# Performance work log

Measured on AMD Instinct MI355X. Metric: run time of the kernel, lower is better.

Reference implementation:

```python
import jax, jax.numpy as jnp
import numpy as np


def setup_inputs() -> dict:
    key = jax.random.key(0)
    kq, kk, kv = jax.random.split(key, 3)
    B, H, S, D = 2, 8, 4096, 64
    return {
        "query": jax.random.normal(kq, (B, H, S, D), dtype=jnp.float32),
        "key": jax.random.normal(kk, (B, H, S, D), dtype=jnp.float32),
        "value": jax.random.normal(kv, (B, H, S, D), dtype=jnp.float32),
    }


def reference(query, key, value):
    # NOTE: the torch source overwrites sqrt(d) with d, so the divisor is D, not sqrt(D).
    d = query.shape[-1]
    # score: [B, H, S_q, S_k]
    score = jnp.einsum("bhqd,bhkd->bhqk", query, key) / d
    relu = jax.nn.relu(score)  # no softmax / row normalization
    out = jnp.einsum("bhqk,bhkd->bhqd", relu, value)
    return out
```

## Files before the change

### kernel.cpp

```cpp
#include <hip/hip_runtime.h>
#include <hip/hip_bf16.h>
#include <stdint.h>


#define NH 16
#define SEQ 4096
#define DD 64
#define HE (SEQ*DD)
#define HB (HE*2)
#define Q16_OFF 0
#define K16_OFF (NH*HB)
#define V16_OFF (2*NH*HB)
#define WS_NEED (3*NH*HB)

typedef __attribute__((ext_vector_type(8)))  short    bf16x8;
typedef __attribute__((ext_vector_type(16))) float    f32x16;
typedef __attribute__((ext_vector_type(4)))  uint32_t u32x4;

__device__ inline uint32_t f2bf1(float f) {
  return (uint32_t)__builtin_bit_cast(unsigned short, __float2bfloat16(f));
}
__device__ inline uint32_t pack2bf(float a, float b) {
  return f2bf1(a) | (f2bf1(b) << 16);
}
__device__ inline uint32_t relu2(uint32_t w) {
  uint32_t r;
  asm("v_pk_max_f16 %0, %1, 0" : "=v"(r) : "v"(w));
  return r;
}

__global__ __launch_bounds__(256) void prepass_kernel(const float* __restrict__ Q,
                                                      const float* __restrict__ K,
                                                      const float* __restrict__ V,
                                                      char* __restrict__ ws) {
  __shared__ float vt[64*65];
  int bx = blockIdx.x, tid = threadIdx.x;
  if (bx < 2048) {
    size_t base = ((size_t)bx*256 + tid)*8;
    const float4* s = (const float4*)(Q + base);
    float4 a = s[0], b = s[1];
    const float sc = 1.0f/64.0f;
    u32x4 o;
    o.x = pack2bf(a.x*sc, a.y*sc);
    o.y = pack2bf(a.z*sc, a.w*sc);
    o.z = pack2bf(b.x*sc, b.y*sc);
    o.w = pack2bf(b.z*sc, b.w*sc);
    *(u32x4*)(ws + Q16_OFF + base*2) = o;
  } else if (bx < 3072) {
    int tile = bx - 2048;
    int head = tile >> 6, t = tile & 63;
    int r = tid >> 2, c0 = (tid & 3) * 16;
    const float4* s4 = (const float4*)(K + (size_t)head*HE + ((size_t)(t*64 + r))*64 + c0);
    float4 f0 = s4[0], f1 = s4[1], f2 = s4[2], f3 = s4[3];
    u32x4 c_lo, c_hi;
    c_lo.x = pack2bf(f0.x, f0.y); c_lo.y = pack2bf(f0.z, f0.w);
    c_lo.z = pack2bf(f1.x, f1.y); c_lo.w = pack2bf(f1.z, f1.w);
    c_hi.x = pack2bf(f2.x, f2.y); c_hi.y = pack2bf(f2.z, f2.w);
    c_hi.z = pack2bf(f3.x, f3.y); c_hi.w = pack2bf(f3.z, f3.w);
    char* tb = ws + K16_OFF + ((size_t)head*64 + t)*8192;
    int sw = (r & 7) << 4;
    *(u32x4*)(tb + r*128 + ((c0*2)      ^ sw)) = c_lo;
    *(u32x4*)(tb + r*128 + ((c0*2 + 16) ^ sw)) = c_hi;
  } else {
    int tile = bx - 3072;
    int head = tile >> 6, t = tile & 63;
    int k = tid >> 2, c0 = (tid & 3)*16;
    const float4* s4 = (const float4*)(V + (size_t)head*HE + ((size_t)(t*64 + k))*64 + c0);
    float4 f0 = s4[0], f1 = s4[1], f2 = s4[2], f3 = s4[3];
    float tmp[16] = {f0.x,f0.y,f0.z,f0.w, f1.x,f1.y,f1.z,f1.w,
                     f2.x,f2.y,f2.z,f2.w, f3.x,f3.y,f3.z,f3.w};
    #pragma unroll
    for (int j = 0; j < 16; ++j) vt[k*65 + c0 + j] = tmp[j];
    __syncthreads();
    int d = tid >> 2, k0 = (tid & 3)*16;
    float v2[16];
    #pragma unroll
    for (int j = 0; j < 16; ++j) v2[j] = vt[(k0 + j)*65 + d];
    u32x4 c_lo, c_hi;
    c_lo.x = pack2bf(v2[0],  v2[1]);  c_lo.y = pack2bf(v2[2],  v2[3]);
    c_lo.z = pack2bf(v2[4],  v2[5]);  c_lo.w = pack2bf(v2[6],  v2[7]);
    c_hi.x = pack2bf(v2[8],  v2[9]);  c_hi.y = pack2bf(v2[10], v2[11]);
    c_hi.z = pack2bf(v2[12], v2[13]); c_hi.w = pack2bf(v2[14], v2[15]);
    char* tb = ws + V16_OFF + ((size_t)head*64 + t)*8192;
    int sw = (d & 7) << 4;
    *(u32x4*)(tb + d*128 + ((k0*2)      ^ sw)) = c_lo;
    *(u32x4*)(tb + d*128 + ((k0*2 + 16) ^ sw)) = c_hi;
  }
}

__global__ __launch_bounds__(512, 4) void attn_kernel(const char* __restrict__ ws,
                                                      float* __restrict__ out) {
  __shared__ __align__(16) char lds[2*2*16384];
  int bx = blockIdx.x;
  int head = bx >> 5, qblk = bx & 31;
  int tid = threadIdx.x;
  int lane = tid & 63, w = tid >> 6;
  int l31 = lane & 31, h = lane >> 5;
  int g  = w >> 2;
  int wq = w & 3;
  int t2 = tid & 255;

  const char* q16 = ws + Q16_OFF + (size_t)head*HB;
  const char* k16 = ws + K16_OFF + (size_t)head*HB;
  const char* v16 = ws + V16_OFF + (size_t)head*HB;
  int qrow0 = qblk*128 + wq*32;

  bf16x8 qf[4];
  #pragma unroll
  for (int t = 0; t < 4; ++t)
    qf[t] = *(const bf16x8*)(q16 + ((size_t)(qrow0 + l31)*64 + t*16 + h*8)*2);

  f32x16 kZero;
  #pragma unroll
  for (int i = 0; i < 16; ++i) kZero[i] = 0.f;

  f32x16 o[2];
  #pragma unroll
  for (int nd = 0; nd < 2; ++nd)
    #pragma unroll
    for (int i = 0; i < 16; ++i) o[nd][i] = 0.f;

  char* ldsg = lds + g*32768;

  auto stage = [&](int cur, int kt) {
    const char* ktile = k16 + (size_t)(g*32 + kt)*8192;
    const char* vtile = v16 + (size_t)(g*32 + kt)*8192;
    char* lk = ldsg + cur*16384;
    char* lv = lk + 8192;
    #pragma unroll
    for (int c = 0; c < 2; ++c) {
      int off = c*4096 + t2*16;
      __builtin_amdgcn_global_load_lds(
          (const __attribute__((address_space(1))) void*)(ktile + off),
          (__attribute__((address_space(3))) void*)(lk + off), 16, 0, 0);
      __builtin_amdgcn_global_load_lds(
          (const __attribute__((address_space(1))) void*)(vtile + off),
          (__attribute__((address_space(3))) void*)(lv + off), 16, 0, 0);
    }
  };

  auto compute = [&](int cur) {
    const char* lk = ldsg + cur*16384;
    const char* lv = lk + 8192;
    f32x16 st[2];
    #pragma unroll
    for (int n = 0; n < 2; ++n) {
      bf16x8 kf[4];
      int row = n*32 + l31;
      int sw = (row & 7) << 4;
      #pragma unroll
      for (int t = 0; t < 4; ++t)
        kf[t] = *(const bf16x8*)(lk + row*128 + ((t*32 + h*16) ^ sw));
      __builtin_amdgcn_s_setprio(1);
      f32x16 acc = __builtin_amdgcn_mfma_f32_32x32x16_bf16(kf[0], qf[0], kZero, 0, 0, 0);
      #pragma unroll
      for (int t = 1; t < 4; ++t)
        acc = __builtin_amdgcn_mfma_f32_32x32x16_bf16(kf[t], qf[t], acc, 0, 0, 0);
      st[n] = acc;
      __builtin_amdgcn_s_setprio(0);
    }
    bf16x8 vf[2][4];
    #pragma unroll
    for (int nd = 0; nd < 2; ++nd) {
      int row = nd*32 + l31;
      int sw = (row & 7) << 4;
      #pragma unroll
      for (int ks = 0; ks < 4; ++ks)
        vf[nd][ks] = *(const bf16x8*)(lv + row*128 + ((ks*32 + h*16) ^ sw));
    }
    bf16x8 pa[4];
    #pragma unroll
    for (int n = 0; n < 2; ++n)
      #pragma unroll
      for (int kn = 0; kn < 2; ++kn) {
        uint32_t a0 = pack2bf(st[n][kn*8+0], st[n][kn*8+1]);
        uint32_t b0 = pack2bf(st[n][kn*8+2], st[n][kn*8+3]);
        uint32_t a2 = pack2bf(st[n][kn*8+4], st[n][kn*8+5]);
        uint32_t b2 = pack2bf(st[n][kn*8+6], st[n][kn*8+7]);
        asm("v_permlane32_swap_b32 %0, %1" : "+v"(a0), "+v"(a2));
        asm("v_permlane32_swap_b32 %0, %1" : "+v"(b0), "+v"(b2));
        union { uint32_t u[4]; bf16x8 v; } pk;
        pk.u[0] = relu2(a0);
        pk.u[1] = relu2(b0);
        pk.u[2] = relu2(a2);
        pk.u[3] = relu2(b2);
        pa[n*2 + kn] = pk.v;
      }
    __builtin_amdgcn_s_setprio(1);
    #pragma unroll
    for (int nd = 0; nd < 2; ++nd)
      #pragma unroll
      for (int ks = 0; ks < 4; ++ks)
        o[nd] = __builtin_amdgcn_mfma_f32_32x32x16_bf16(pa[ks], vf[nd][ks], o[nd], 0, 0, 0);
    __builtin_amdgcn_s_setprio(0);
  };

  stage(0, 0);
  stage(1, 1);
  #pragma unroll 1
  for (int kt = 0; kt < 30; ++kt) {
    int cur = kt & 1;
    asm volatile("s_waitcnt vmcnt(4)" ::: "memory");
    __builtin_amdgcn_s_barrier();
    __builtin_amdgcn_sched_barrier(0);
    compute(cur);
    __builtin_amdgcn_sched_barrier(0);
    __builtin_amdgcn_s_barrier();
    stage(cur, kt + 2);
  }
  asm volatile("s_waitcnt vmcnt(4)" ::: "memory");
  __builtin_amdgcn_s_barrier();
  __builtin_amdgcn_sched_barrier(0);
  compute(0);
  __builtin_amdgcn_sched_barrier(0);
  __builtin_amdgcn_s_barrier();
  asm volatile("s_waitcnt vmcnt(0)" ::: "memory");
  __builtin_amdgcn_s_barrier();
  __builtin_amdgcn_sched_barrier(0);
  compute(1);

  __syncthreads();
  float* red = (float*)lds;
  if (g == 1) {
    #pragma unroll
    for (int nd = 0; nd < 2; ++nd)
      #pragma unroll
      for (int r = 0; r < 16; ++r) {
        int ql = wq*32 + (r & 3) + 8*(r >> 2) + 4*h;
        red[ql*64 + nd*32 + l31] = o[nd][r];
      }
  }
  __syncthreads();
  if (g == 0) {
    float* outh = out + (size_t)head*HE;
    #pragma unroll
    for (int nd = 0; nd < 2; ++nd)
      #pragma unroll
      for (int r = 0; r < 16; ++r) {
        int ql = wq*32 + (r & 3) + 8*(r >> 2) + 4*h;
        float v = o[nd][r] + red[ql*64 + nd*32 + l31];
        outh[(size_t)(qblk*128 + ql)*64 + nd*32 + l31] = v;
      }
  }
}

extern "C" void kernel_launch(void* const* d_in, const int* in_sizes, int n_in,
                              void* d_out, int out_size, void* d_ws, size_t ws_size,
                              hipStream_t stream) {
  if (n_in < 3 || ws_size < (size_t)WS_NEED) return;
  const float* Q = (const float*)d_in[0];
  const float* K = (const float*)d_in[1];
  const float* V = (const float*)d_in[2];
  float* out = (float*)d_out;
  char* ws = (char*)d_ws;
  hipLaunchKernelGGL(prepass_kernel, dim3(4096), dim3(256), 0, stream, Q, K, V, ws);
  hipLaunchKernelGGL(attn_kernel,    dim3(512),  dim3(512), 0, stream, ws, out);
}
```

Measured before the change: 87.59 us.

## Load V fragments directly from global and single-buffer K through LDS

The attention kernel now reads V fragments straight from global memory into registers instead of staging them through LDS, and K is staged with a one-ahead double buffer that waits on vmcnt(0) each iteration. This halves LDS usage, which could raise occupancy and cut LDS traffic. Two smaller changes ride along: the bf16 conversion uses the packed v_cvt_pk_bf16_f32 instruction, and block IDs are remapped so that neighbouring blocks spread across heads. The prepass stops swizzling V to match the direct global reads. The risk is exposed global latency on the V loads and a shallower prefetch for K.

New measurement: 183.2 us. 2.09x slower.

```diff
diff --git a/kernel.cpp b/kernel.cpp
--- a/kernel.cpp
+++ b/kernel.cpp
@@ -22,6 +22,11 @@
 }
 __device__ inline uint32_t pack2bf(float a, float b) {
   return f2bf1(a) | (f2bf1(b) << 16);
+}
+__device__ inline uint32_t cvtpk(float lo, float hi) {
+  uint32_t r;
+  asm("v_cvt_pk_bf16_f32 %0, %1, %2" : "=v"(r) : "v"(lo), "v"(hi));
+  return r;
 }
 __device__ inline uint32_t relu2(uint32_t w) {
   uint32_t r;
@@ -82,28 +87,27 @@
     c_hi.x = pack2bf(v2[8],  v2[9]);  c_hi.y = pack2bf(v2[10], v2[11]);
     c_hi.z = pack2bf(v2[12], v2[13]); c_hi.w = pack2bf(v2[14], v2[15]);
     char* tb = ws + V16_OFF + ((size_t)head*64 + t)*8192;
-    int sw = (d & 7) << 4;
-    *(u32x4*)(tb + d*128 + ((k0*2)      ^ sw)) = c_lo;
-    *(u32x4*)(tb + d*128 + ((k0*2 + 16) ^ sw)) = c_hi;
+    *(u32x4*)(tb + d*128 + k0*2)        = c_lo;
+    *(u32x4*)(tb + d*128 + (k0*2 + 16)) = c_hi;
   }
 }
 
 __global__ __launch_bounds__(512, 4) void attn_kernel(const char* __restrict__ ws,
                                                       float* __restrict__ out) {
-  __shared__ __align__(16) char lds[2*2*16384];
-  int bx = blockIdx.x;
+  __shared__ __align__(16) char lds[2*2*8192];
+  int bid = blockIdx.x;
+  int bx = (bid & 7) * 64 + (bid >> 3);
   int head = bx >> 5, qblk = bx & 31;
   int tid = threadIdx.x;
   int lane = tid & 63, w = tid >> 6;
   int l31 = lane & 31, h = lane >> 5;
   int g  = w >> 2;
-  int wq = w & 3;
-  int t2 = tid & 255;
+  int wg = w & 3;
 
   const char* q16 = ws + Q16_OFF + (size_t)head*HB;
   const char* k16 = ws + K16_OFF + (size_t)head*HB;
   const char* v16 = ws + V16_OFF + (size_t)head*HB;
-  int qrow0 = qblk*128 + wq*32;
+  int qrow0 = qblk*128 + wg*32;
 
   bf16x8 qf[4];
   #pragma unroll
@@ -120,28 +124,39 @@
     #pragma unroll
     for (int i = 0; i < 16; ++i) o[nd][i] = 0.f;
 
-  char* ldsg = lds + g*32768;
-
   auto stage = [&](int cur, int kt) {
     const char* ktile = k16 + (size_t)(g*32 + kt)*8192;
-    const char* vtile = v16 + (size_t)(g*32 + kt)*8192;
-    char* lk = ldsg + cur*16384;
-    char* lv = lk + 8192;
+    char* lk = lds + (g*2 + cur)*8192;
     #pragma unroll
     for (int c = 0; c < 2; ++c) {
-      int off = c*4096 + t2*16;
+      int off = (wg*2 + c)*1024 + lane*16;
       __builtin_amdgcn_global_load_lds(
           (const __attribute__((address_space(1))) void*)(ktile + off),
           (__attribute__((address_space(3))) void*)(lk + off), 16, 0, 0);
-      __builtin_amdgcn_global_load_lds(
-          (const __attribute__((address_space(1))) void*)(vtile + off),
-          (__attribute__((address_space(3))) void*)(lv + off), 16, 0, 0);
     }
   };
 
-  auto compute = [&](int cur) {
-    const char* lk = ldsg + cur*16384;
-    const char* lv = lk + 8192;
+  stage(0, 0);
+  #pragma unroll 1
+  for (int kt = 0; kt < 32; ++kt) {
+    int cur = kt & 1;
+    asm volatile("s_waitcnt vmcnt(0)" ::: "memory");
+    __builtin_amdgcn_s_barrier();
+    __builtin_amdgcn_sched_barrier(0);
+
+    const char* vtile = v16 + (size_t)(g*32 + kt)*8192;
+    bf16x8 vf[2][4];
+    #pragma unroll
+    for (int nd = 0; nd < 2; ++nd) {
+      int row = nd*32 + l31;
+      #pragma unroll
+      for (int ks = 0; ks < 4; ++ks)
+        vf[nd][ks] = *(const bf16x8*)(vtile + row*128 + ks*32 + h*16);
+    }
+
+    stage(cur ^ 1, (kt + 1) & 31);
+
+    const char* lk = lds + (g*2 + cur)*8192;
     f32x16 st[2];
     #pragma unroll
     for (int n = 0; n < 2; ++n) {
@@ -159,33 +174,26 @@
       st[n] = acc;
       __builtin_amdgcn_s_setprio(0);
     }
-    bf16x8 vf[2][4];
-    #pragma unroll
-    for (int nd = 0; nd < 2; ++nd) {
-      int row = nd*32 + l31;
-      int sw = (row & 7) << 4;
-      #pragma unroll
-      for (int ks = 0; ks < 4; ++ks)
-        vf[nd][ks] = *(const bf16x8*)(lv + row*128 + ((ks*32 + h*16) ^ sw));
-    }
+
     bf16x8 pa[4];
     #pragma unroll
     for (int n = 0; n < 2; ++n)
       #pragma unroll
       for (int kn = 0; kn < 2; ++kn) {
-        uint32_t a0 = pack2bf(st[n][kn*8+0], st[n][kn*8+1]);
-        uint32_t b0 = pack2bf(st[n][kn*8+2], st[n][kn*8+3]);
-        uint32_t a2 = pack2bf(st[n][kn*8+4], st[n][kn*8+5]);
-        uint32_t b2 = pack2bf(st[n][kn*8+6], st[n][kn*8+7]);
-        asm("v_permlane32_swap_b32 %0, %1" : "+v"(a0), "+v"(a2));
-        asm("v_permlane32_swap_b32 %0, %1" : "+v"(b0), "+v"(b2));
+        uint32_t w0 = cvtpk(st[n][kn*8+0], st[n][kn*8+1]);
+        uint32_t w1 = cvtpk(st[n][kn*8+2], st[n][kn*8+3]);
+        uint32_t w2 = cvtpk(st[n][kn*8+4], st[n][kn*8+5]);
+        uint32_t w3 = cvtpk(st[n][kn*8+6], st[n][kn*8+7]);
+        asm("v_permlane32_swap_b32 %0, %1" : "+v"(w0), "+v"(w2));
+        asm("v_permlane32_swap_b32 %0, %1" : "+v"(w1), "+v"(w3));
         union { uint32_t u[4]; bf16x8 v; } pk;
-        pk.u[0] = relu2(a0);
-        pk.u[1] = relu2(b0);
-        pk.u[2] = relu2(a2);
-        pk.u[3] = relu2(b2);
+        pk.u[0] = relu2(w0);
+        pk.u[1] = relu2(w1);
+        pk.u[2] = relu2(w2);
+        pk.u[3] = relu2(w3);
         pa[n*2 + kn] = pk.v;
       }
+
     __builtin_amdgcn_s_setprio(1);
     #pragma unroll
     for (int nd = 0; nd < 2; ++nd)
@@ -193,31 +201,7 @@
       for (int ks = 0; ks < 4; ++ks)
         o[nd] = __builtin_amdgcn_mfma_f32_32x32x16_bf16(pa[ks], vf[nd][ks], o[nd], 0, 0, 0);
     __builtin_amdgcn_s_setprio(0);
-  };
-
-  stage(0, 0);
-  stage(1, 1);
-  #pragma unroll 1
-  for (int kt = 0; kt < 30; ++kt) {
-    int cur = kt & 1;
-    asm volatile("s_waitcnt vmcnt(4)" ::: "memory");
-    __builtin_amdgcn_s_barrier();
-    __builtin_amdgcn_sched_barrier(0);
-    compute(cur);
-    __builtin_amdgcn_sched_barrier(0);
-    __builtin_amdgcn_s_barrier();
-    stage(cur, kt + 2);
-  }
-  asm volatile("s_waitcnt vmcnt(4)" ::: "memory");
-  __builtin_amdgcn_s_barrier();
-  __builtin_amdgcn_sched_barrier(0);
-  compute(0);
-  __builtin_amdgcn_sched_barrier(0);
-  __builtin_amdgcn_s_barrier();
-  asm volatile("s_waitcnt vmcnt(0)" ::: "memory");
-  __builtin_amdgcn_s_barrier();
-  __builtin_amdgcn_sched_barrier(0);
-  compute(1);
+  }
 
   __syncthreads();
   float* red = (float*)lds;
@@ -226,7 +210,7 @@
     for (int nd = 0; nd < 2; ++nd)
       #pragma unroll
       for (int r = 0; r < 16; ++r) {
-        int ql = wq*32 + (r & 3) + 8*(r >> 2) + 4*h;
+        int ql = wg*32 + (r & 3) + 8*(r >> 2) + 4*h;
         red[ql*64 + nd*32 + l31] = o[nd][r];
       }
   }
@@ -237,7 +221,7 @@
     for (int nd = 0; nd < 2; ++nd)
       #pragma unroll
       for (int r = 0; r < 16; ++r) {
-        int ql = wq*32 + (r & 3) + 8*(r >> 2) + 4*h;
+        int ql = wg*32 + (r & 3) + 8*(r >> 2) + 4*h;
         float v = o[nd][r] + red[ql*64 + nd*32 + l31];
         outh[(size_t)(qblk*128 + ql)*64 + nd*32 + l31] = v;
       }
```
